# Optimization experiments

Measured on AMD Instinct MI355X. Metric: run time of the kernel, lower is better.

## Reference

```python
import jax, jax.numpy as jnp
import numpy as np

D_MODEL = 1024
N_HEADS = 16
D_FF = 4096
WINDOW = 256
EPS = 1e-5


def setup_inputs() -> dict:
    key = jax.random.key(0)
    ks = jax.random.split(key, 12)
    B, T, C = 4, 1024, D_MODEL
    s = lambda fan: 1.0 / np.sqrt(fan)
    return {
        "x": jax.random.normal(ks[0], (B, T, C), jnp.float32),
        "Wqkv": jax.random.normal(ks[1], (3 * C, C), jnp.float32) * s(C),
        "bqkv": jnp.zeros((3 * C,), jnp.float32),
        "Wo": jax.random.normal(ks[2], (C, C), jnp.float32) * s(C),
        "bo": jnp.zeros((C,), jnp.float32),
        "W1": jax.random.normal(ks[3], (D_FF, C), jnp.float32) * s(C),
        "b1": jnp.zeros((D_FF,), jnp.float32),
        "W2": jax.random.normal(ks[4], (C, D_FF), jnp.float32) * s(D_FF),
        "b2": jnp.zeros((C,), jnp.float32),
        "g1": jnp.ones((C,), jnp.float32),
        "be1": jnp.zeros((C,), jnp.float32),
        "g2": jnp.ones((C,), jnp.float32),
        "be2": jnp.zeros((C,), jnp.float32),
    }


def _layernorm(x, g, b):
    mu = jnp.mean(x, axis=-1, keepdims=True)
    var = jnp.mean(jnp.square(x - mu), axis=-1, keepdims=True)
    return (x - mu) * jax.lax.rsqrt(var + EPS) * g + b


def reference(x, Wqkv, bqkv, Wo, bo, W1, b1, W2, b2, g1, be1, g2, be2):
    B, T, C = x.shape
    H, Dh = N_HEADS, C // N_HEADS
    # QKV projection (torch MultiheadAttention packed in_proj)
    qkv = jnp.einsum("btc,ec->bte", x, Wqkv) + bqkv  # [B,T,3C]
    q, k, v = jnp.split(qkv, 3, axis=-1)
    q = q.reshape(B, T, H, Dh).transpose(0, 2, 1, 3)  # [B,H,T,Dh]
    k = k.reshape(B, T, H, Dh).transpose(0, 2, 1, 3)
    v = v.reshape(B, T, H, Dh).transpose(0, 2, 1, 3)
    scores = jnp.einsum("bhqd,bhkd->bhqk", q, k) / jnp.sqrt(jnp.float32(Dh))
    # causal banded mask: key j visible to query i iff 0 <= i-j < WINDOW
    i = jnp.arange(T)[:, None]
    j = jnp.arange(T)[None, :]
    band = (j <= i) & (i - j < WINDOW)
    scores = jnp.where(band, scores, -jnp.inf)
    attn = jax.nn.softmax(scores, axis=-1)
    ctx = jnp.einsum("bhqk,bhkd->bhqd", attn, v)  # [B,H,T,Dh]
    ctx = ctx.transpose(0, 2, 1, 3).reshape(B, T, C)
    attn_out = jnp.einsum("btc,oc->bto", ctx, Wo) + bo
    x = _layernorm(x + attn_out, g1, be1)
    h = jax.nn.gelu(jnp.einsum("btc,fc->btf", x, W1) + b1, approximate=False)
    ffn_out = jnp.einsum("btf,cf->btc", h, W2) + b2
    return _layernorm(x + ffn_out, g2, be2)
```

## Files before the change

### kernel.cpp

```cpp
#include <hip/hip_runtime.h>
#include <hip/hip_bf16.h>

typedef __attribute__((ext_vector_type(4))) float floatx4;
typedef __attribute__((ext_vector_type(8))) short shortx8;

struct bf4 { __hip_bfloat16 h[4]; };
union U8 { shortx8 v; __hip_bfloat16 h[8]; };
union U4 { unsigned long long v; __hip_bfloat16 h[4]; };

__device__ __forceinline__ void async_copy16(const __hip_bfloat16* g, __hip_bfloat16* l) {
  __builtin_amdgcn_global_load_lds((__attribute__((address_space(1))) void*)g,
                                   (__attribute__((address_space(3))) void*)l,
                                   16, 0, 0);
}

__global__ __launch_bounds__(256) void cast_all_kernel(
    const float* __restrict__ s0, __hip_bfloat16* __restrict__ d0, int nb0,
    const float* __restrict__ s1, __hip_bfloat16* __restrict__ d1, int nb1,
    const float* __restrict__ s2, __hip_bfloat16* __restrict__ d2, int nb2,
    const float* __restrict__ s3, __hip_bfloat16* __restrict__ d3, int nb3,
    const float* __restrict__ s4, __hip_bfloat16* __restrict__ d4) {
  int b = blockIdx.x;
  const float* src; __hip_bfloat16* dst;
  if (b < nb0) { src = s0; dst = d0; }
  else { b -= nb0;
    if (b < nb1) { src = s1; dst = d1; }
    else { b -= nb1;
      if (b < nb2) { src = s2; dst = d2; }
      else { b -= nb2;
        if (b < nb3) { src = s3; dst = d3; }
        else { b -= nb3; src = s4; dst = d4; }
      }
    }
  }
  const int i = b * 256 + threadIdx.x;
  const float4 v = ((const float4*)src)[i];
  bf4 o4;
  o4.h[0] = __float2bfloat16(v.x);
  o4.h[1] = __float2bfloat16(v.y);
  o4.h[2] = __float2bfloat16(v.z);
  o4.h[3] = __float2bfloat16(v.w);
  *(bf4*)(dst + (size_t)i * 4) = o4;
}

#define STG_A(slot, kt, ks)                                                    \
  async_copy16(Ag + (size_t)(kt) * 64 + (size_t)(ks) * 32,                     \
               &As[slot][tid * 8]);                                            \
  async_copy16(Ag + (size_t)128 * K + (size_t)(kt) * 64 + (size_t)(ks) * 32,   \
               &As[slot][4096 + tid * 8]);

#define STG_B(slot, kt, ks)                                                    \
  async_copy16(Bg + (size_t)(kt) * 64 + (size_t)(ks) * 32,                     \
               &Bs[slot][tid * 8]);                                            \
  async_copy16(Bg + (size_t)128 * K + (size_t)(kt) * 64 + (size_t)(ks) * 32,   \
               &Bs[slot][4096 + tid * 8]);

#define G256_READ_A(dst, slot, mh)                                             \
  _Pragma("unroll")                                                            \
  for (int i_ = 0; i_ < 4; ++i_)                                               \
    dst[i_] = *(const shortx8*)&As[slot][ard + ((mh) * 4 + i_) * 512];

#define G256_READ_B(dst, slot)                                                 \
  _Pragma("unroll")                                                            \
  for (int i_ = 0; i_ < 4; ++i_)                                               \
    dst[i_] = *(const shortx8*)&Bs[slot][brd + i_ * 512];

#define G256_MFMA(afr, bfr, MH)                                                \
  __builtin_amdgcn_sched_barrier(0);                                           \
  __builtin_amdgcn_s_setprio(1);                                               \
  _Pragma("unroll")                                                            \
  for (int mi_ = 0; mi_ < 4; ++mi_)                                            \
    _Pragma("unroll")                                                          \
    for (int ni_ = 0; ni_ < 4; ++ni_)                                          \
      acc[(MH) * 4 + mi_][ni_] = __builtin_amdgcn_mfma_f32_16x16x32_bf16(      \
          afr[mi_], bfr[ni_], acc[(MH) * 4 + mi_][ni_], 0, 0, 0);              \
  __builtin_amdgcn_s_setprio(0);                                               \
  __builtin_amdgcn_sched_barrier(0);

#define G256_BAR() asm volatile("s_barrier" ::: "memory")

#define G256_KLOOP()                                                           \
  STG_A(0, 0, 0) STG_B(0, 0, 0)                                                \
  STG_A(1, 0, 1) STG_B(1, 0, 1)                                                \
  STG_A(2, 1, 0) STG_B(2, 1, 0)                                                \
  asm volatile("s_waitcnt vmcnt(8)" ::: "memory");                             \
  G256_BAR();                                                                  \
  shortx8 a0[4], a1[4], bE[4], bO[4];                                          \
  G256_READ_B(bE, 0)                                                           \
  G256_READ_A(a0, 0, 0)                                                        \
  for (int T = 0; T < NKT; ++T) {                                              \
    const int s00 = (2 * T) & 3;                                               \
    const int s01 = (2 * T + 1) & 3;                                           \
    const int sx  = (2 * T + 2) & 3;                           \
    const int sn1 = (2 * T + 3) & 3;                           \
    const int sn0 = (2 * T + 4) & 3;                           \
    const bool st1 = (T + 1 < NKT);                                            \
    const bool st2 = (T + 2 < NKT);                                            \
                                                                       \
    G256_BAR();                                                                \
    if (st1) { asm volatile("s_waitcnt vmcnt(4)" ::: "memory"); }              \
    else     { asm volatile("s_waitcnt vmcnt(0)" ::: "memory"); }              \
    G256_READ_A(a1, s00, 1)                                                    \
    if (st1) { STG_A(sn1, T + 1, 1) }                                          \
    G256_MFMA(a0, bE, 0)                                                       \
                                                                       \
    G256_BAR();                                                                \
    G256_READ_B(bO, s01)                                                       \
    G256_READ_A(a0, s01, 0)                                                    \
    if (st1) { STG_B(sn1, T + 1, 1) }                                          \
    G256_MFMA(a1, bE, 1)                                                       \
                                                                       \
    G256_BAR();                                                                \
    if (st1) { asm volatile("s_waitcnt vmcnt(4)" ::: "memory"); }              \
    else     { asm volatile("s_waitcnt vmcnt(0)" ::: "memory"); }              \
    G256_READ_A(a1, s01, 1)                                                    \
    if (st2) { STG_A(sn0, T + 2, 0) }                                          \
    G256_MFMA(a0, bO, 0)                                                       \
                                                                       \
    G256_BAR();                                                                \
    if (st1) {                                                                 \
      G256_READ_B(bE, sx)                                                      \
      G256_READ_A(a0, sx, 0)                                                   \
    }                                                                          \
    if (st2) { STG_B(sn0, T + 2, 0) }                                          \
    G256_MFMA(a1, bO, 1)                                                       \
  }

template<int EPI>
__global__ __launch_bounds__(512, 2) void gemm256(
    const __hip_bfloat16* __restrict__ A,
    const __hip_bfloat16* __restrict__ B,
    const float* __restrict__ bias,
    __hip_bfloat16* __restrict__ outb,
    int M, int N, int K, int NT)
{
  __shared__ __align__(16) __hip_bfloat16 As[4][256 * 32];
  __shared__ __align__(16) __hip_bfloat16 Bs[4][256 * 32];
  const int tid  = threadIdx.x;
  const int lane = tid & 63;
  const int wave = tid >> 6;
  const int wr = wave >> 2;
  const int wc = wave & 3;
  const int fr = lane & 15;
  const int fq = lane >> 4;

  const int nwg = gridDim.x;
  const int cpx = nwg >> 3;
  const int swz = (blockIdx.x & 7) * cpx + (blockIdx.x >> 3);
  const int mt = swz / NT, nt = swz % NT;
  const long bm = (long)mt * 256, bn = (long)nt * 256;

  const int srow = tid >> 2;
  const int sch  = (tid & 3) ^ ((tid >> 3) & 3);
  const __hip_bfloat16* Ag = A + (bm + srow) * (size_t)K + sch * 8;
  const __hip_bfloat16* Bg = B + (bn + srow) * (size_t)K + sch * 8;

  const int swc = (fq ^ ((fr >> 1) & 3)) << 3;
  const int ard = (wr * 128 + fr) * 32 + swc;
  const int brd = (wc * 64 + fr) * 32 + swc;

  const floatx4 zero = {0.f, 0.f, 0.f, 0.f};
  floatx4 acc[8][4];
#pragma unroll
  for (int mi = 0; mi < 8; ++mi)
#pragma unroll
    for (int ni = 0; ni < 4; ++ni) acc[mi][ni] = zero;

  const int NKT = K >> 6;
  G256_KLOOP()

#pragma unroll
  for (int mi = 0; mi < 8; ++mi) {
#pragma unroll
    for (int ni = 0; ni < 4; ++ni) {
      const long col = bn + wc * 64 + ni * 16 + fr;
      const float bv = bias[col];
#pragma unroll
      for (int r = 0; r < 4; ++r) {
        const long row = bm + wr * 128 + mi * 16 + fq * 4 + r;
        float v = acc[mi][ni][r] + bv;
        if (EPI == 1) {
          const float u = v + 0.044715f * v * v * v;
          v = v / (1.0f + __expf(-1.5957691216057308f * u));
        }
        outb[(size_t)row * N + col] = __float2bfloat16(v);
      }
    }
  }
}

__global__ __launch_bounds__(512, 2) void gemm256_splitk(
    const __hip_bfloat16* __restrict__ A,
    const __hip_bfloat16* __restrict__ B,
    __hip_bfloat16* __restrict__ part,
    int M, int N, int K, int Klen, int NT, int TPS)
{
  __shared__ __align__(16) __hip_bfloat16 As[4][256 * 32];
  __shared__ __align__(16) __hip_bfloat16 Bs[4][256 * 32];
  const int tid  = threadIdx.x;
  const int lane = tid & 63;
  const int wave = tid >> 6;
  const int wr = wave >> 2;
  const int wc = wave & 3;
  const int fr = lane & 15;
  const int fq = lane >> 4;

  const int nwg = gridDim.x;
  const int cpx = nwg >> 3;
  const int swz = (blockIdx.x & 7) * cpx + (blockIdx.x >> 3);
  const int zt = swz / TPS;
  const int tile = swz % TPS;
  const int mt = tile / NT, nt = tile % NT;
  const long bm = (long)mt * 256, bn = (long)nt * 256;
  const int kstart = zt * Klen;

  const int srow = tid >> 2;
  const int sch  = (tid & 3) ^ ((tid >> 3) & 3);
  const __hip_bfloat16* Ag = A + (bm + srow) * (size_t)K + kstart + sch * 8;
  const __hip_bfloat16* Bg = B + (bn + srow) * (size_t)K + kstart + sch * 8;

  const int swc = (fq ^ ((fr >> 1) & 3)) << 3;
  const int ard = (wr * 128 + fr) * 32 + swc;
  const int brd = (wc * 64 + fr) * 32 + swc;

  const floatx4 zero = {0.f, 0.f, 0.f, 0.f};
  floatx4 acc[8][4];
#pragma unroll
  for (int mi = 0; mi < 8; ++mi)
#pragma unroll
    for (int ni = 0; ni < 4; ++ni) acc[mi][ni] = zero;

  const int NKT = Klen >> 6;
  G256_KLOOP()

  __hip_bfloat16* outp = part + (size_t)zt * M * N;
#pragma unroll
  for (int mi = 0; mi < 8; ++mi) {
#pragma unroll
    for (int ni = 0; ni < 4; ++ni) {
      const long col = bn + wc * 64 + ni * 16 + fr;
#pragma unroll
      for (int r = 0; r < 4; ++r) {
        const long row = bm + wr * 128 + mi * 16 + fq * 4 + r;
        outp[(size_t)row * N + col] = __float2bfloat16(acc[mi][ni][r]);
      }
    }
  }
}

__global__ __launch_bounds__(256) void transpose_v_kernel(
    const __hip_bfloat16* __restrict__ qkv, __hip_bfloat16* __restrict__ vt)
{
  const int bh = blockIdx.y;
  const int tt = blockIdx.x;
  const int b = bh >> 4, h = bh & 15;
  __shared__ __hip_bfloat16 tile[64][65];
  const int tid = threadIdx.x;
  const int r = tid >> 2;
  const int c = (tid & 3) << 4;
  const __hip_bfloat16* src = qkv + (size_t)(b * 1024 + tt * 64 + r) * 3072 + 2048 + h * 64 + c;
  U8 u0, u1;
  u0.v = *(const shortx8*)src;
  u1.v = *(const shortx8*)(src + 8);
#pragma unroll
  for (int j = 0; j < 8; ++j) { tile[r][c + j] = u0.h[j]; tile[r][c + 8 + j] = u1.h[j]; }
  __syncthreads();
  U8 w0, w1;
#pragma unroll
  for (int j = 0; j < 8; ++j) { w0.h[j] = tile[c + j][r]; w1.h[j] = tile[c + 8 + j][r]; }
  __hip_bfloat16* dst = vt + ((size_t)bh * 64 + r) * 1024 + tt * 64 + c;
  *(shortx8*)dst       = w0.v;
  *(shortx8*)(dst + 8) = w1.v;
}

__global__ __launch_bounds__(256) void attn_kernel(
    const __hip_bfloat16* __restrict__ qkv,
    const __hip_bfloat16* __restrict__ vt,
    __hip_bfloat16* __restrict__ ctx)
{
  const int wave = threadIdx.x >> 6;
  const int lane = threadIdx.x & 63;
  const int gw = blockIdx.x * 4 + wave;
  const int qt = gw & 63;
  const int bh = gw >> 6;
  const int b = bh >> 4, h = bh & 15;
  const int fr = lane & 15, fq = lane >> 4;
  const int q0 = qt << 4;

  __shared__ __align__(16) __hip_bfloat16 Plds[4][16 * 32];
  __hip_bfloat16* Pw = Plds[wave];

  const __hip_bfloat16* qrow = qkv + (size_t)(b * 1024 + q0 + fr) * 3072 + h * 64;
  const shortx8 aq0 = *(const shortx8*)(qrow + fq * 8);
  const shortx8 aq1 = *(const shortx8*)(qrow + 32 + fq * 8);

  const float SC = 0.125f * 1.44269504088896f;
  float m_r[4] = {-1e30f, -1e30f, -1e30f, -1e30f};
  float l_r[4] = {0.f, 0.f, 0.f, 0.f};
  const floatx4 zero = {0.f, 0.f, 0.f, 0.f};
  floatx4 o[4];
#pragma unroll
  for (int nd = 0; nd < 4; ++nd) o[nd] = zero;

  const int kt0 = (q0 >= 255) ? ((q0 - 255) >> 5) : 0;
  const int kt1 = (q0 + 15) >> 5;
  for (int kt = kt0; kt <= kt1; ++kt) {
    const int kbase = kt << 5;
    const __hip_bfloat16* krow0 = qkv + (size_t)(b * 1024 + kbase + fr) * 3072 + 1024 + h * 64;
    const __hip_bfloat16* krow1 = krow0 + 16 * 3072;
    const shortx8 bk00 = *(const shortx8*)(krow0 + fq * 8);
    const shortx8 bk01 = *(const shortx8*)(krow0 + 32 + fq * 8);
    const shortx8 bk10 = *(const shortx8*)(krow1 + fq * 8);
    const shortx8 bk11 = *(const shortx8*)(krow1 + 32 + fq * 8);
    floatx4 s0 = zero, s1 = zero;
    s0 = __builtin_amdgcn_mfma_f32_16x16x32_bf16(aq0, bk00, s0, 0, 0, 0);
    s0 = __builtin_amdgcn_mfma_f32_16x16x32_bf16(aq1, bk01, s0, 0, 0, 0);
    s1 = __builtin_amdgcn_mfma_f32_16x16x32_bf16(aq0, bk10, s1, 0, 0, 0);
    s1 = __builtin_amdgcn_mfma_f32_16x16x32_bf16(aq1, bk11, s1, 0, 0, 0);
#pragma unroll
    for (int r = 0; r < 4; ++r) { s0[r] *= SC; s1[r] *= SC; }
    if (kbase + 31 > q0 || kbase < q0 - 240) {
#pragma unroll
      for (int r = 0; r < 4; ++r) {
        const int tq = q0 + fq * 4 + r;
        const int j0 = kbase + fr;
        const int j1 = j0 + 16;
        if (j0 > tq || j0 < tq - 255) s0[r] = -3e38f;
        if (j1 > tq || j1 < tq - 255) s1[r] = -3e38f;
      }
    }
#pragma unroll
    for (int r = 0; r < 4; ++r) {
      float vmax = fmaxf(s0[r], s1[r]);
      vmax = fmaxf(vmax, __shfl_xor(vmax, 1));
      vmax = fmaxf(vmax, __shfl_xor(vmax, 2));
      vmax = fmaxf(vmax, __shfl_xor(vmax, 4));
      vmax = fmaxf(vmax, __shfl_xor(vmax, 8));
      const float mnew = fmaxf(m_r[r], vmax);
      const float alpha = exp2f(m_r[r] - mnew);
      const float p0 = exp2f(s0[r] - mnew);
      const float p1 = exp2f(s1[r] - mnew);
      m_r[r] = mnew;
      float ps = p0 + p1;
      ps += __shfl_xor(ps, 1);
      ps += __shfl_xor(ps, 2);
      ps += __shfl_xor(ps, 4);
      ps += __shfl_xor(ps, 8);
      l_r[r] = l_r[r] * alpha + ps;
      o[0][r] *= alpha; o[1][r] *= alpha; o[2][r] *= alpha; o[3][r] *= alpha;
      Pw[(fq * 4 + r) * 32 + fr]      = __float2bfloat16(p0);
      Pw[(fq * 4 + r) * 32 + 16 + fr] = __float2bfloat16(p1);
    }
    asm volatile("s_waitcnt lgkmcnt(0)" ::: "memory");
    const shortx8 ap = *(const shortx8*)&Pw[fr * 32 + fq * 8];
#pragma unroll
    for (int nd = 0; nd < 4; ++nd) {
      const shortx8 bv = *(const shortx8*)&vt[((size_t)bh * 64 + nd * 16 + fr) * 1024 + kbase + fq * 8];
      o[nd] = __builtin_amdgcn_mfma_f32_16x16x32_bf16(ap, bv, o[nd], 0, 0, 0);
    }
    asm volatile("s_waitcnt lgkmcnt(0)" ::: "memory");
  }
#pragma unroll
  for (int nd = 0; nd < 4; ++nd)
#pragma unroll
    for (int r = 0; r < 4; ++r)
      ctx[(size_t)(b * 1024 + q0 + fq * 4 + r) * 1024 + h * 64 + nd * 16 + fr] =
          __float2bfloat16(o[nd][r] / l_r[r]);
}

template<int S, int WB>
__global__ __launch_bounds__(256) void ln_sum_kernel(
    const __hip_bfloat16* __restrict__ part,
    const float* __restrict__ resid,
    const float* __restrict__ bias,
    const float* __restrict__ g, const float* __restrict__ be,
    float* __restrict__ outf, __hip_bfloat16* __restrict__ outb)
{
  const int row = blockIdx.x;
  const int tid = threadIdx.x;
  const size_t base = (size_t)row * 1024;
  float4 v = ((const float4*)(resid + base))[tid];
  const float4 bv = ((const float4*)bias)[tid];
  v.x += bv.x; v.y += bv.y; v.z += bv.z; v.w += bv.w;
#pragma unroll
  for (int s = 0; s < S; ++s) {
    U4 p;
    p.v = *(const unsigned long long*)&part[(size_t)s * 4096 * 1024 + base + tid * 4];
    v.x += __bfloat162float(p.h[0]);
    v.y += __bfloat162float(p.h[1]);
    v.z += __bfloat162float(p.h[2]);
    v.w += __bfloat162float(p.h[3]);
  }
  float sm = v.x + v.y + v.z + v.w;
  float ss = v.x * v.x + v.y * v.y + v.z * v.z + v.w * v.w;
#pragma unroll
  for (int off = 1; off < 64; off <<= 1) {
    sm += __shfl_xor(sm, off);
    ss += __shfl_xor(ss, off);
  }
  __shared__ float red[8];
  if ((tid & 63) == 0) { red[tid >> 6] = sm; red[4 + (tid >> 6)] = ss; }
  __syncthreads();
  sm = red[0] + red[1] + red[2] + red[3];
  ss = red[4] + red[5] + red[6] + red[7];
  const float mu = sm * (1.0f / 1024.0f);
  const float rs = rsqrtf(ss * (1.0f / 1024.0f) - mu * mu + 1e-5f);
  const float4 gg = ((const float4*)g)[tid];
  const float4 bb = ((const float4*)be)[tid];
  float4 y;
  y.x = (v.x - mu) * rs * gg.x + bb.x;
  y.y = (v.y - mu) * rs * gg.y + bb.y;
  y.z = (v.z - mu) * rs * gg.z + bb.z;
  y.w = (v.w - mu) * rs * gg.w + bb.w;
  ((float4*)(outf + base))[tid] = y;
  if (WB) {
    bf4 o4;
    o4.h[0] = __float2bfloat16(y.x);
    o4.h[1] = __float2bfloat16(y.y);
    o4.h[2] = __float2bfloat16(y.z);
    o4.h[3] = __float2bfloat16(y.w);
    *(bf4*)(outb + base + tid * 4) = o4;
  }
}

extern "C" void kernel_launch(void* const* d_in, const int* in_sizes, int n_in,
                              void* d_out, int out_size, void* d_ws, size_t ws_size,
                              hipStream_t stream) {
  const float* x    = (const float*)d_in[0];
  const float* Wqkv = (const float*)d_in[1];
  const float* bqkv = (const float*)d_in[2];
  const float* Wo   = (const float*)d_in[3];
  const float* bo   = (const float*)d_in[4];
  const float* W1   = (const float*)d_in[5];
  const float* b1   = (const float*)d_in[6];
  const float* W2   = (const float*)d_in[7];
  const float* b2   = (const float*)d_in[8];
  const float* g1   = (const float*)d_in[9];
  const float* be1  = (const float*)d_in[10];
  const float* g2   = (const float*)d_in[11];
  const float* be2  = (const float*)d_in[12];

  char* ws = (char*)d_ws;
  size_t off = 0;
  auto alloc = [&](size_t bytes) -> void* {
    void* p = ws + off;
    off += (bytes + 255) & ~(size_t)255;
    return p;
  };
  __hip_bfloat16* wqkvb = (__hip_bfloat16*)alloc(6291456);
  __hip_bfloat16* wob   = (__hip_bfloat16*)alloc(2097152);
  __hip_bfloat16* w1b   = (__hip_bfloat16*)alloc(8388608);
  __hip_bfloat16* w2b   = (__hip_bfloat16*)alloc(8388608);
  __hip_bfloat16* xb    = (__hip_bfloat16*)alloc(8388608);
  __hip_bfloat16* qkvb  = (__hip_bfloat16*)alloc(25165824);
  __hip_bfloat16* vtb   = (__hip_bfloat16*)alloc(8388608);
  __hip_bfloat16* ctxb  = (__hip_bfloat16*)alloc(8388608);
  __hip_bfloat16* part  = (__hip_bfloat16*)alloc(4u * 8388608);
  float*          x1f   = (float*)alloc(16777216);
  __hip_bfloat16* x1b   = (__hip_bfloat16*)alloc(8388608);
  __hip_bfloat16* hb    = (__hip_bfloat16*)alloc(33554432);
  (void)ws_size; (void)in_sizes; (void)n_in; (void)out_size;

  cast_all_kernel<<<16384, 256, 0, stream>>>(x, xb, 4096,
                                             Wqkv, wqkvb, 3072,
                                             Wo, wob, 1024,
                                             W1, w1b, 4096,
                                             W2, w2b);
  gemm256<0><<<192, 512, 0, stream>>>(xb, wqkvb, bqkv, qkvb, 4096, 3072, 1024, 12);
  transpose_v_kernel<<<dim3(16, 64), 256, 0, stream>>>(qkvb, vtb);
  attn_kernel<<<1024, 256, 0, stream>>>(qkvb, vtb, ctxb);
  gemm256_splitk<<<256, 512, 0, stream>>>(ctxb, wob, part, 4096, 1024, 1024, 256, 4, 64);
  ln_sum_kernel<4, 1><<<4096, 256, 0, stream>>>(part, x, bo, g1, be1, x1f, x1b);
  gemm256<1><<<256, 512, 0, stream>>>(x1b, w1b, b1, hb, 4096, 4096, 1024, 16);
  gemm256_splitk<<<256, 512, 0, stream>>>(hb, w2b, part, 4096, 1024, 4096, 1024, 4, 64);
  ln_sum_kernel<4, 0><<<4096, 256, 0, stream>>>(part, x1f, b2, g2, be2, (float*)d_out, nullptr);
}
```

Before: 321.4 us.

## Rework 256x256 GEMMs to 16 waves with four-slot half-K pipeline

```diff
diff --git a/kernel.cpp b/kernel.cpp
--- a/kernel.cpp
+++ b/kernel.cpp
@@ -43,91 +43,59 @@
   *(bf4*)(dst + (size_t)i * 4) = o4;
 }
 
-#define STG_A(slot, kt, ks)                                                    \
-  async_copy16(Ag + (size_t)(kt) * 64 + (size_t)(ks) * 32,                     \
-               &As[slot][tid * 8]);                                            \
-  async_copy16(Ag + (size_t)128 * K + (size_t)(kt) * 64 + (size_t)(ks) * 32,   \
-               &As[slot][4096 + tid * 8]);
-
-#define STG_B(slot, kt, ks)                                                    \
-  async_copy16(Bg + (size_t)(kt) * 64 + (size_t)(ks) * 32,                     \
-               &Bs[slot][tid * 8]);                                            \
-  async_copy16(Bg + (size_t)128 * K + (size_t)(kt) * 64 + (size_t)(ks) * 32,   \
-               &Bs[slot][4096 + tid * 8]);
-
-#define G256_READ_A(dst, slot, mh)                                             \
-  _Pragma("unroll")                                                            \
-  for (int i_ = 0; i_ < 4; ++i_)                                               \
-    dst[i_] = *(const shortx8*)&As[slot][ard + ((mh) * 4 + i_) * 512];
-
-#define G256_READ_B(dst, slot)                                                 \
-  _Pragma("unroll")                                                            \
-  for (int i_ = 0; i_ < 4; ++i_)                                               \
-    dst[i_] = *(const shortx8*)&Bs[slot][brd + i_ * 512];
-
-#define G256_MFMA(afr, bfr, MH)                                                \
-  __builtin_amdgcn_sched_barrier(0);                                           \
-  __builtin_amdgcn_s_setprio(1);                                               \
-  _Pragma("unroll")                                                            \
-  for (int mi_ = 0; mi_ < 4; ++mi_)                                            \
+#define G5_VM(n)   asm volatile("s_waitcnt vmcnt(" #n ")" ::: "memory")
+#define G5_BAR()   asm volatile("s_barrier" ::: "memory")
+#define G5_LGKM0() asm volatile("s_waitcnt lgkmcnt(0)" ::: "memory")
+#define G5_SB()    __builtin_amdgcn_sched_barrier(0)
+
+#define G5_STAGE(slot, koff)                                                   \
+  async_copy16(Ag + (koff), &As[slot][tid * 8]);                               \
+  async_copy16(Bg + (koff), &Bs[slot][tid * 8]);
+
+#define G5_PHASE(slot, SOFF, DOSTG, VMW)                                       \
+  {                                                                            \
+    shortx8 fa[4], fb[4];                                                      \
     _Pragma("unroll")                                                          \
-    for (int ni_ = 0; ni_ < 4; ++ni_)                                          \
-      acc[(MH) * 4 + mi_][ni_] = __builtin_amdgcn_mfma_f32_16x16x32_bf16(      \
-          afr[mi_], bfr[ni_], acc[(MH) * 4 + mi_][ni_], 0, 0, 0);              \
-  __builtin_amdgcn_s_setprio(0);                                               \
-  __builtin_amdgcn_sched_barrier(0);
-
-#define G256_BAR() asm volatile("s_barrier" ::: "memory")
-
-#define G256_KLOOP()                                                           \
-  STG_A(0, 0, 0) STG_B(0, 0, 0)                                                \
-  STG_A(1, 0, 1) STG_B(1, 0, 1)                                                \
-  STG_A(2, 1, 0) STG_B(2, 1, 0)                                                \
-  asm volatile("s_waitcnt vmcnt(8)" ::: "memory");                             \
-  G256_BAR();                                                                  \
-  shortx8 a0[4], a1[4], bE[4], bO[4];                                          \
-  G256_READ_B(bE, 0)                                                           \
-  G256_READ_A(a0, 0, 0)                                                        \
-  for (int T = 0; T < NKT; ++T) {                                              \
-    const int s00 = (2 * T) & 3;                                               \
-    const int s01 = (2 * T + 1) & 3;                                           \
-    const int sx  = (2 * T + 2) & 3;                           \
-    const int sn1 = (2 * T + 3) & 3;                           \
-    const int sn0 = (2 * T + 4) & 3;                           \
-    const bool st1 = (T + 1 < NKT);                                            \
-    const bool st2 = (T + 2 < NKT);                                            \
-                                                                       \
-    G256_BAR();                                                                \
-    if (st1) { asm volatile("s_waitcnt vmcnt(4)" ::: "memory"); }              \
-    else     { asm volatile("s_waitcnt vmcnt(0)" ::: "memory"); }              \
-    G256_READ_A(a1, s00, 1)                                                    \
-    if (st1) { STG_A(sn1, T + 1, 1) }                                          \
-    G256_MFMA(a0, bE, 0)                                                       \
-                                                                       \
-    G256_BAR();                                                                \
-    G256_READ_B(bO, s01)                                                       \
-    G256_READ_A(a0, s01, 0)                                                    \
-    if (st1) { STG_B(sn1, T + 1, 1) }                                          \
-    G256_MFMA(a1, bE, 1)                                                       \
-                                                                       \
-    G256_BAR();                                                                \
-    if (st1) { asm volatile("s_waitcnt vmcnt(4)" ::: "memory"); }              \
-    else     { asm volatile("s_waitcnt vmcnt(0)" ::: "memory"); }              \
-    G256_READ_A(a1, s01, 1)                                                    \
-    if (st2) { STG_A(sn0, T + 2, 0) }                                          \
-    G256_MFMA(a0, bO, 0)                                                       \
-                                                                       \
-    G256_BAR();                                                                \
-    if (st1) {                                                                 \
-      G256_READ_B(bE, sx)                                                      \
-      G256_READ_A(a0, sx, 0)                                                   \
-    }                                                                          \
-    if (st2) { STG_B(sn0, T + 2, 0) }                                          \
-    G256_MFMA(a1, bO, 1)                                                       \
-  }
+    for (int i_ = 0; i_ < 4; ++i_)                                             \
+      fa[i_] = *(const shortx8*)&As[slot][ard + i_ * 512];                     \
+    _Pragma("unroll")                                                          \
+    for (int i_ = 0; i_ < 4; ++i_)                                             \
+      fb[i_] = *(const shortx8*)&Bs[slot][brd + i_ * 512];                     \
+    if (DOSTG) { G5_STAGE((((slot) + 3) & 3), SOFF) }                          \
+    VMW;                                                                       \
+    G5_BAR();                                                                  \
+    G5_LGKM0(); G5_SB();                                                       \
+    __builtin_amdgcn_s_setprio(1);                                             \
+    _Pragma("unroll")                                                          \
+    for (int mi_ = 0; mi_ < 4; ++mi_)                                          \
+      _Pragma("unroll")                                                        \
+      for (int ni_ = 0; ni_ < 4; ++ni_)                                        \
+        acc[mi_][ni_] = __builtin_amdgcn_mfma_f32_16x16x32_bf16(               \
+            fa[mi_], fb[ni_], acc[mi_][ni_], 0, 0, 0);                         \
+    __builtin_amdgcn_s_setprio(0);                                             \
+    G5_SB();                                                                   \
+    G5_BAR();                                                                  \
+  }
+
+#define G5_KLOOP()                                                             \
+  G5_STAGE(0, 0) G5_STAGE(1, 32) G5_STAGE(2, 64)                               \
+  G5_VM(4); G5_BAR();                                                          \
+  const int NITER = (NH - 4) >> 2;                                             \
+  _Pragma("clang loop unroll(disable)")                                        \
+  for (int it = 0; it < NITER; ++it) {                                         \
+    G5_PHASE(0, 96,  true, G5_VM(4))                                           \
+    G5_PHASE(1, 128, true, G5_VM(4))                                           \
+    G5_PHASE(2, 160, true, G5_VM(4))                                           \
+    G5_PHASE(3, 192, true, G5_VM(4))                                           \
+    Ag += 128; Bg += 128;                                                      \
+  }                                                                            \
+  G5_PHASE(0, 96, true, G5_VM(4))                                              \
+  G5_PHASE(1, 0, false, G5_VM(2))                                              \
+  G5_PHASE(2, 0, false, G5_VM(0))                                              \
+  G5_PHASE(3, 0, false, (void)0)
 
 template<int EPI>
-__global__ __launch_bounds__(512, 2) void gemm256(
+__global__ __launch_bounds__(1024, 4) void gemm256(
     const __hip_bfloat16* __restrict__ A,
     const __hip_bfloat16* __restrict__ B,
     const float* __restrict__ bias,
@@ -156,28 +124,28 @@
   const __hip_bfloat16* Bg = B + (bn + srow) * (size_t)K + sch * 8;
 
   const int swc = (fq ^ ((fr >> 1) & 3)) << 3;
-  const int ard = (wr * 128 + fr) * 32 + swc;
+  const int ard = (wr * 64 + fr) * 32 + swc;
   const int brd = (wc * 64 + fr) * 32 + swc;
 
   const floatx4 zero = {0.f, 0.f, 0.f, 0.f};
-  floatx4 acc[8][4];
-#pragma unroll
-  for (int mi = 0; mi < 8; ++mi)
+  floatx4 acc[4][4];
+#pragma unroll
+  for (int mi = 0; mi < 4; ++mi)
 #pragma unroll
     for (int ni = 0; ni < 4; ++ni) acc[mi][ni] = zero;
 
-  const int NKT = K >> 6;
-  G256_KLOOP()
-
-#pragma unroll
-  for (int mi = 0; mi < 8; ++mi) {
+  const int NH = K >> 5;
+  G5_KLOOP()
+
+#pragma unroll
+  for (int mi = 0; mi < 4; ++mi) {
 #pragma unroll
     for (int ni = 0; ni < 4; ++ni) {
       const long col = bn + wc * 64 + ni * 16 + fr;
       const float bv = bias[col];
 #pragma unroll
       for (int r = 0; r < 4; ++r) {
-        const long row = bm + wr * 128 + mi * 16 + fq * 4 + r;
+        const long row = bm + wr * 64 + mi * 16 + fq * 4 + r;
         float v = acc[mi][ni][r] + bv;
         if (EPI == 1) {
           const float u = v + 0.044715f * v * v * v;
@@ -189,7 +157,7 @@
   }
 }
 
-__global__ __launch_bounds__(512, 2) void gemm256_splitk(
+__global__ __launch_bounds__(1024, 4) void gemm256_splitk(
     const __hip_bfloat16* __restrict__ A,
     const __hip_bfloat16* __restrict__ B,
     __hip_bfloat16* __restrict__ part,
@@ -220,28 +188,28 @@
   const __hip_bfloat16* Bg = B + (bn + srow) * (size_t)K + kstart + sch * 8;
 
   const int swc = (fq ^ ((fr >> 1) & 3)) << 3;
-  const int ard = (wr * 128 + fr) * 32 + swc;
+  const int ard = (wr * 64 + fr) * 32 + swc;
   const int brd = (wc * 64 + fr) * 32 + swc;
 
   const floatx4 zero = {0.f, 0.f, 0.f, 0.f};
-  floatx4 acc[8][4];
-#pragma unroll
-  for (int mi = 0; mi < 8; ++mi)
+  floatx4 acc[4][4];
+#pragma unroll
+  for (int mi = 0; mi < 4; ++mi)
 #pragma unroll
     for (int ni = 0; ni < 4; ++ni) acc[mi][ni] = zero;
 
-  const int NKT = Klen >> 6;
-  G256_KLOOP()
+  const int NH = Klen >> 5;
+  G5_KLOOP()
 
   __hip_bfloat16* outp = part + (size_t)zt * M * N;
 #pragma unroll
-  for (int mi = 0; mi < 8; ++mi) {
+  for (int mi = 0; mi < 4; ++mi) {
 #pragma unroll
     for (int ni = 0; ni < 4; ++ni) {
       const long col = bn + wc * 64 + ni * 16 + fr;
 #pragma unroll
       for (int r = 0; r < 4; ++r) {
-        const long row = bm + wr * 128 + mi * 16 + fq * 4 + r;
+        const long row = bm + wr * 64 + mi * 16 + fq * 4 + r;
         outp[(size_t)row * N + col] = __float2bfloat16(acc[mi][ni][r]);
       }
     }
@@ -466,12 +434,12 @@
                                              Wo, wob, 1024,
                                              W1, w1b, 4096,
                                              W2, w2b);
-  gemm256<0><<<192, 512, 0, stream>>>(xb, wqkvb, bqkv, qkvb, 4096, 3072, 1024, 12);
+  gemm256<0><<<192, 1024, 0, stream>>>(xb, wqkvb, bqkv, qkvb, 4096, 3072, 1024, 12);
   transpose_v_kernel<<<dim3(16, 64), 256, 0, stream>>>(qkvb, vtb);
   attn_kernel<<<1024, 256, 0, stream>>>(qkvb, vtb, ctxb);
-  gemm256_splitk<<<256, 512, 0, stream>>>(ctxb, wob, part, 4096, 1024, 1024, 256, 4, 64);
+  gemm256_splitk<<<256, 1024, 0, stream>>>(ctxb, wob, part, 4096, 1024, 1024, 256, 4, 64);
   ln_sum_kernel<4, 1><<<4096, 256, 0, stream>>>(part, x, bo, g1, be1, x1f, x1b);
-  gemm256<1><<<256, 512, 0, stream>>>(x1b, w1b, b1, hb, 4096, 4096, 1024, 16);
-  gemm256_splitk<<<256, 512, 0, stream>>>(hb, w2b, part, 4096, 1024, 4096, 1024, 4, 64);
+  gemm256<1><<<256, 1024, 0, stream>>>(x1b, w1b, b1, hb, 4096, 4096, 1024, 16);
+  gemm256_splitk<<<256, 1024, 0, stream>>>(hb, w2b, part, 4096, 1024, 4096, 1024, 4, 64);
   ln_sum_kernel<4, 0><<<4096, 256, 0, stream>>>(part, x1f, b2, g2, be2, (float*)d_out, nullptr);
 }
```

Result: no change. 324.3 us (+0.9%).
